# Kernel tuning notes

Hardware: AMD Instinct MI355X
Metric: run time of the kernel (lower is better)

Reference implementation:

```python
import jax, jax.numpy as jnp
import numpy as np

NUM_HEADS = 8


def _mha(x, w_in, b_in, w_out, b_out, nh=NUM_HEADS):
    # x: [B, L, H]; torch nn.MultiheadAttention (batch_first) self-attention
    B, L, H = x.shape
    dh = H // nh
    qkv = x @ w_in.T + b_in                      # [B, L, 3H]
    q, k, v = jnp.split(qkv, 3, axis=-1)
    def heads(t):
        return t.reshape(B, L, nh, dh).transpose(0, 2, 1, 3)  # [B, nh, L, dh]
    q, k, v = heads(q), heads(k), heads(v)
    scale = 1.0 / np.sqrt(dh)
    scores = jnp.einsum('bhqd,bhkd->bhqk', q * scale, k)      # [B, nh, L, L]
    attn = jax.nn.softmax(scores, axis=-1)
    out = jnp.einsum('bhqk,bhkd->bhqd', attn, v)               # [B, nh, L, dh]
    out = out.transpose(0, 2, 1, 3).reshape(B, L, H)
    return out @ w_out.T + b_out


def setup_inputs() -> dict:
    key = jax.random.key(0)
    ks = jax.random.split(key, 10)
    S, M, B, H = 64, 4, 128, 1024
    std = 0.02
    inp = {
        'hidden_states_combined': jax.random.normal(ks[0], (S, M, B, 1, H), jnp.float32),
        'mf_in_w': jax.random.normal(ks[1], (3 * H, H), jnp.float32) * std,
        'mf_in_b': jnp.zeros((3 * H,), jnp.float32),
        'mf_out_w': jax.random.normal(ks[2], (H, H), jnp.float32) * std,
        'mf_out_b': jnp.zeros((H,), jnp.float32),
        'sf_in_w': jax.random.normal(ks[3], (3 * H, H), jnp.float32) * std,
        'sf_in_b': jnp.zeros((3 * H,), jnp.float32),
        'sf_out_w': jax.random.normal(ks[4], (H, H), jnp.float32) * std,
        'sf_out_b': jnp.zeros((H,), jnp.float32),
        'pos_enc': jax.random.normal(ks[5], (1, S, H), jnp.float32) * std,
    }
    return inp


def reference(hidden_states_combined, mf_in_w, mf_in_b, mf_out_w, mf_out_b,
              sf_in_w, sf_in_b, sf_out_w, sf_out_b, pos_enc):
    S, M, B, _, H = hidden_states_combined.shape
    # [S, M, B, 1, H] -> [S, B, M, H] -> batch all steps together: [S*B, M, H]
    x = hidden_states_combined[:, :, :, 0, :].transpose(0, 2, 1, 3).reshape(S * B, M, H)
    fused = _mha(x, mf_in_w, mf_in_b, mf_out_w, mf_out_b)        # [S*B, M, H]
    fused = fused.mean(axis=1).reshape(S, B, H)                  # mean over models
    seq = fused.transpose(1, 0, 2) + pos_enc[:, :S, :]            # [B, S, H]
    enhanced = _mha(seq, sf_in_w, sf_in_b, sf_out_w, sf_out_b)   # [B, S, H]
    return enhanced.transpose(1, 0, 2)[:, :, None, :]             # [S, B, 1, H]
```

## Files before the change

### kernel.cpp

```cpp
#include <hip/hip_runtime.h>

typedef unsigned short u16;
typedef __attribute__((ext_vector_type(8))) short bf16x8;
typedef __attribute__((ext_vector_type(4))) float f32x4;

__device__ __forceinline__ u16 f2bf(float f) {
  unsigned u = __float_as_uint(f);
  u += 0x7FFFu + ((u >> 16) & 1u);
  return (u16)(u >> 16);
}
__device__ __forceinline__ float bf2f(u16 h) {
  return __uint_as_float(((unsigned)h) << 16);
}

#define GLOAD16(g, l) __builtin_amdgcn_global_load_lds( \
    (const __attribute__((address_space(1))) void*)(g), \
    (__attribute__((address_space(3))) void*)(l), 16, 0, 0)

__global__ __launch_bounds__(256) void cvtw4_kernel(const float* __restrict__ s0, u16* __restrict__ d0,
                                                    const float* __restrict__ s1, u16* __restrict__ d1,
                                                    const float* __restrict__ s2, u16* __restrict__ d2,
                                                    const float* __restrict__ s3, u16* __restrict__ d3) {
  int i = blockIdx.x * 256 + threadIdx.x;
  const float* s; u16* d; int off;
  if (i < 786432)       { s = s0; d = d0; off = i; }
  else if (i < 1048576) { s = s1; d = d1; off = i - 786432; }
  else if (i < 1835008) { s = s2; d = d2; off = i - 1048576; }
  else                  { s = s3; d = d3; off = i - 1835008; }
  float4 f = ((const float4*)s)[off];
  ushort4 u;
  u.x = f2bf(f.x); u.y = f2bf(f.y); u.z = f2bf(f.z); u.w = f2bf(f.w);
  ((ushort4*)d)[off] = u;
}

__global__ __launch_bounds__(256) void xcvt_kernel(const float* __restrict__ hidden,
                                                   u16* __restrict__ xb, int s0) {
  int idx = blockIdx.x * 256 + threadIdx.x;
  int h4 = idx & 255;
  int lrow = idx >> 8;
  int m = lrow & 3;
  int b = (lrow >> 2) & 127;
  int sl = lrow >> 9;
  int s = s0 + sl;
  const float4 f = *(const float4*)(hidden + (((size_t)(s * 4 + m) * 128 + b) * 1024) + h4 * 4);
  ushort4 u;
  u.x = f2bf(f.x); u.y = f2bf(f.y); u.z = f2bf(f.z); u.w = f2bf(f.w);
  *(ushort4*)(xb + (size_t)lrow * 1024 + h4 * 4) = u;
}

template <int KK>
__global__ __launch_bounds__(512, 2) void gemm4p(const u16* __restrict__ A,
                                                 const u16* __restrict__ Bw,
                                                 const float* __restrict__ bias,
                                                 u16* __restrict__ C, int N) {
  __shared__ u16 Sh[65536];
  const int t = threadIdx.x, w = t >> 6, l = t & 63;
  const int lr = l & 15, lg = l >> 4;
  const int wm = w >> 2, wn = w & 3;

  const int gx = gridDim.x;
  const int nb = gx * gridDim.y;
  const int id = blockIdx.y * gx + blockIdx.x;
  const int id2 = (id & 7) * (nb >> 3) + (id >> 3);
  const int rowBase = (id2 / gx) * 256, colBase = (id2 % gx) * 256;

  const int sslot8 = ((t & 3) ^ ((t >> 3) & 3)) * 8;
  const u16* Ag = A + (size_t)(rowBase + (t >> 2)) * KK + sslot8;
  const u16* Bg = Bw + (size_t)(colBase + (t >> 2)) * KK + sslot8;
  const size_t K128 = (size_t)128 * KK;
  const int ldsW = w * 512;

  const int fslot8 = (lg ^ ((lr >> 1) & 3)) * 8;
  const int aRowOff = (wm * 128 + lr) * 32 + fslot8;
  const int bRowOff = (wn * 64 + lr) * 32 + fslot8;

  f32x4 acc[8][4];
#pragma unroll
  for (int i = 0; i < 8; i++)
#pragma unroll
    for (int j = 0; j < 4; j++) acc[i][j] = (f32x4){0.f, 0.f, 0.f, 0.f};
  bf16x8 af[2][8], bfr[2][4];

#define STGA(tt, KH, DB) { \
    const u16* g_ = Ag + (size_t)(tt) * 64 + (KH) * 32; \
    GLOAD16(g_, Sh + ((DB) * 2 + (KH)) * 8192 + ldsW); \
    GLOAD16(g_ + K128, Sh + ((DB) * 2 + (KH)) * 8192 + 4096 + ldsW); }
#define STGB(tt, KH, DB) { \
    const u16* g_ = Bg + (size_t)(tt) * 64 + (KH) * 32; \
    GLOAD16(g_, Sh + 32768 + ((DB) * 2 + (KH)) * 8192 + ldsW); \
    GLOAD16(g_ + K128, Sh + 32768 + ((DB) * 2 + (KH)) * 8192 + 4096 + ldsW); }

#define RA8(DD, KH, BUF) { \
    const u16* sa_ = Sh + ((DD) * 2 + (KH)) * 8192 + aRowOff; \
    _Pragma("unroll") \
    for (int mi = 0; mi < 8; mi++) af[BUF][mi] = *(const bf16x8*)(sa_ + mi * 512); }
#define RB4(DD, KH, BUF) { \
    const u16* sb_ = Sh + 32768 + ((DD) * 2 + (KH)) * 8192 + bRowOff; \
    _Pragma("unroll") \
    for (int n = 0; n < 4; n++) bfr[BUF][n] = *(const bf16x8*)(sb_ + n * 512); }

#define LG(NN) asm volatile("s_waitcnt lgkmcnt(" #NN ")" ::: "memory"); \
               __builtin_amdgcn_sched_barrier(0)
#define WTC(NN) asm volatile("s_waitcnt vmcnt(" #NN ")" ::: "memory")
#define BAR asm volatile("s_barrier" ::: "memory")

#define MM32(BUF) { \
    __builtin_amdgcn_s_setprio(1); \
    _Pragma("unroll") \
    for (int mi = 0; mi < 8; mi++) { \
      _Pragma("unroll") \
      for (int n = 0; n < 4; n++) \
        acc[mi][n] = __builtin_amdgcn_mfma_f32_16x16x32_bf16( \
            af[BUF][mi], bfr[BUF][n], acc[mi][n], 0, 0, 0); \
    } \
    __builtin_amdgcn_s_setprio(0); }

  STGA(0, 0, 0); STGB(0, 0, 0);
  STGA(0, 1, 0); STGB(0, 1, 0);
  STGA(1, 0, 1); STGB(1, 0, 1);
  WTC(4);
  BAR;
  RA8(0, 0, 0); RB4(0, 0, 0);

  const int nt = KK / 64;
  for (int tt = 0; tt < nt; ++tt) {
    const int dd = tt & 1;
    RA8(dd, 1, 1); RB4(dd, 1, 1);
    if (tt + 1 < nt) { STGA(tt + 1, 1, dd ^ 1); STGB(tt + 1, 1, dd ^ 1); }
    LG(12);
    MM32(0);
    if (tt + 1 < nt) { WTC(4); }
    BAR;
    if (tt + 1 < nt) {
      RA8(dd ^ 1, 0, 0); RB4(dd ^ 1, 0, 0);
      if (tt + 2 < nt) { STGA(tt + 2, 0, dd); STGB(tt + 2, 0, dd); }
      LG(12);
    } else {
      LG(0);
    }
    MM32(1);
    if (tt + 2 < nt) { WTC(4); }
    else if (tt + 1 < nt) { WTC(0); }
    BAR;
  }
#undef MM32
#undef BAR
#undef WTC
#undef LG
#undef RB4
#undef RA8
#undef STGB
#undef STGA

  const int orow0 = rowBase + wm * 128 + lg * 4;
  const int ocol0 = colBase + wn * 64 + lr;
#pragma unroll
  for (int m = 0; m < 8; m++) {
#pragma unroll
    for (int n = 0; n < 4; n++) {
      const int col = ocol0 + n * 16;
      const float bv = bias[col];
#pragma unroll
      for (int r = 0; r < 4; r++) {
        const int row = orow0 + m * 16 + r;
        C[(size_t)row * N + col] = f2bf(acc[m][n][r] + bv);
      }
    }
  }
}

template <int MODE>
__global__ __launch_bounds__(256, 2) void gemm_fp(const u16* __restrict__ A,
                                                  const u16* __restrict__ Bw,
                                                  const float* __restrict__ bias,
                                                  void* __restrict__ Cout,
                                                  int N, int K,
                                                  const float* __restrict__ posenc) {
  __shared__ u16 SA[3][8192];
  __shared__ u16 SB[3][4096];
  const int t = threadIdx.x, w = t >> 6, l = t & 63;
  const int lr = l & 15, lg = l >> 4;
  const int wm = w >> 1, wn = w & 1;

  const int gx = gridDim.x;
  const int nb = gx * gridDim.y;
  const int id = blockIdx.y * gx + blockIdx.x;
  const int id2 = (id & 7) * (nb >> 3) + (id >> 3);
  const int rowBase = (id2 / gx) * 256, colBase = (id2 % gx) * 128;

  const int srow = l >> 2;
  const int ssl = ((l & 3) ^ (srow & 3)) * 8;
  const u16* Ag = A + (size_t)(rowBase + w * 16 + srow) * K + ssl;
  const u16* Bg = Bw + (size_t)(colBase + w * 16 + srow) * K + ssl;
  u16* const lA = &SA[0][0] + w * 512;
  u16* const lB = &SB[0][0] + w * 512;

  const int fsw = (lg ^ (lr & 3)) * 8;
  const int aoff = (wm * 128 + lr) * 32 + fsw;
  const int boff = (wn * 64 + lr) * 32 + fsw;

  f32x4 acc[8][4];
#pragma unroll
  for (int i = 0; i < 8; i++)
#pragma unroll
    for (int j = 0; j < 4; j++) acc[i][j] = (f32x4){0.f, 0.f, 0.f, 0.f};

#define STG_P0(tt, bb) do { \
    const size_t ko_ = (size_t)(tt) * 32; \
    GLOAD16(Ag + ko_,                    lA + (bb) * 8192); \
    GLOAD16(Ag + ko_ + (size_t)64 * K,   lA + (bb) * 8192 + 2048); \
    GLOAD16(Ag + ko_ + (size_t)128 * K,  lA + (bb) * 8192 + 4096); \
  } while (0)
#define STG_P1(tt, bb) do { \
    const size_t ko_ = (size_t)(tt) * 32; \
    GLOAD16(Ag + ko_ + (size_t)192 * K,  lA + (bb) * 8192 + 6144); \
    GLOAD16(Bg + ko_,                    lB + (bb) * 4096); \
    GLOAD16(Bg + ko_ + (size_t)64 * K,   lB + (bb) * 4096 + 2048); \
  } while (0)
#define FBAR asm volatile("s_barrier" ::: "memory")

  const int nt = K >> 5;
  STG_P0(0, 0); STG_P1(0, 0);
  STG_P0(1, 1); STG_P1(1, 1);
  asm volatile("s_waitcnt vmcnt(6)" ::: "memory");
  FBAR;

  int bcur = 0;
  for (int tt = 0; tt < nt; ++tt) {
    const u16* pa = &SA[bcur][0];
    const u16* pb = &SB[bcur][0];
    const int bnext = (bcur + 2 > 2) ? bcur - 1 : bcur + 2;
    bf16x8 af[4], bfr[4];

#pragma unroll
    for (int m = 0; m < 4; m++) af[m] = *(const bf16x8*)(pa + aoff + m * 512);
#pragma unroll
    for (int n = 0; n < 4; n++) bfr[n] = *(const bf16x8*)(pb + boff + n * 512);
    if (tt + 2 < nt) STG_P0(tt + 2, bnext);
    FBAR;
    asm volatile("s_waitcnt lgkmcnt(0)" ::: "memory");
    __builtin_amdgcn_sched_barrier(0);
    __builtin_amdgcn_s_setprio(1);
#pragma unroll
    for (int m = 0; m < 4; m++)
#pragma unroll
      for (int n = 0; n < 4; n++)
        acc[m][n] = __builtin_amdgcn_mfma_f32_16x16x32_bf16(af[m], bfr[n], acc[m][n], 0, 0, 0);
    __builtin_amdgcn_s_setprio(0);
    FBAR;

#pragma unroll
    for (int m = 0; m < 4; m++) af[m] = *(const bf16x8*)(pa + aoff + (m + 4) * 512);
    if (tt + 2 < nt) STG_P1(tt + 2, bnext);
    FBAR;
    asm volatile("s_waitcnt lgkmcnt(0)" ::: "memory");
    __builtin_amdgcn_sched_barrier(0);
    __builtin_amdgcn_s_setprio(1);
#pragma unroll
    for (int m = 0; m < 4; m++)
#pragma unroll
      for (int n = 0; n < 4; n++)
        acc[m + 4][n] = __builtin_amdgcn_mfma_f32_16x16x32_bf16(af[m], bfr[n], acc[m + 4][n], 0, 0, 0);
    __builtin_amdgcn_s_setprio(0);
    if (tt + 2 < nt) {
      asm volatile("s_waitcnt vmcnt(6)" ::: "memory");
    } else if (tt + 1 < nt) {
      asm volatile("s_waitcnt vmcnt(0)" ::: "memory");
    }
    FBAR;
    bcur = (bcur + 1 > 2) ? 0 : bcur + 1;
  }
#undef FBAR
#undef STG_P0
#undef STG_P1

  const int orow0 = rowBase + wm * 128 + lg * 4;
  const int ocol0 = colBase + wn * 64 + lr;
#pragma unroll
  for (int m = 0; m < 8; m++) {
#pragma unroll
    for (int n = 0; n < 4; n++) {
      const int col = ocol0 + n * 16;
      const float bv = bias[col];
#pragma unroll
      for (int r = 0; r < 4; r++) {
        const int row = orow0 + m * 16 + r;
        float v = acc[m][n][r] + bv;
        if (MODE == 1) {
          int s = row >> 7, b = row & 127;
          v += posenc[s * 1024 + col];
          ((u16*)Cout)[((size_t)(b * 64 + s)) * 1024 + col] = f2bf(v);
        } else {
          int s = row & 63, b = row >> 6;
          ((float*)Cout)[((size_t)(s * 128 + b)) * 1024 + col] = v;
        }
      }
    }
  }
}

__global__ __launch_bounds__(256) void attn1_kernel(const u16* __restrict__ qkv,
                                                    u16* __restrict__ am, int seqBase) {
  const int w = threadIdx.x >> 6, l = threadIdx.x & 63;
  const int pair = blockIdx.x * 4 + w;
  const int seq = pair >> 3, head = pair & 7;
  const int d0 = l * 2;
  const u16* base = qkv + (size_t)(seq * 4) * 3072 + head * 128 + d0;
  const float scale = 0.08838834764831845f;
  float q[4][2], k[4][2], v[4][2];
#pragma unroll
  for (int m = 0; m < 4; m++) {
    ushort2 uq = *(const ushort2*)(base + (size_t)m * 3072);
    ushort2 uk = *(const ushort2*)(base + (size_t)m * 3072 + 1024);
    ushort2 uv = *(const ushort2*)(base + (size_t)m * 3072 + 2048);
    q[m][0] = bf2f(uq.x) * scale; q[m][1] = bf2f(uq.y) * scale;
    k[m][0] = bf2f(uk.x);         k[m][1] = bf2f(uk.y);
    v[m][0] = bf2f(uv.x);         v[m][1] = bf2f(uv.y);
  }
  float sc[4][4];
#pragma unroll
  for (int i = 0; i < 4; i++)
#pragma unroll
    for (int j = 0; j < 4; j++)
      sc[i][j] = q[i][0] * k[j][0] + q[i][1] * k[j][1];
#pragma unroll
  for (int off = 32; off >= 1; off >>= 1)
#pragma unroll
    for (int i = 0; i < 4; i++)
#pragma unroll
      for (int j = 0; j < 4; j++)
        sc[i][j] += __shfl_xor(sc[i][j], off, 64);
  float pbar[4] = {0.f, 0.f, 0.f, 0.f};
#pragma unroll
  for (int i = 0; i < 4; i++) {
    float mx = fmaxf(fmaxf(sc[i][0], sc[i][1]), fmaxf(sc[i][2], sc[i][3]));
    float e0 = __expf(sc[i][0] - mx), e1 = __expf(sc[i][1] - mx);
    float e2 = __expf(sc[i][2] - mx), e3 = __expf(sc[i][3] - mx);
    float inv = 0.25f / (e0 + e1 + e2 + e3);
    pbar[0] += e0 * inv; pbar[1] += e1 * inv; pbar[2] += e2 * inv; pbar[3] += e3 * inv;
  }
  float o0 = pbar[0] * v[0][0] + pbar[1] * v[1][0] + pbar[2] * v[2][0] + pbar[3] * v[3][0];
  float o1 = pbar[0] * v[0][1] + pbar[1] * v[1][1] + pbar[2] * v[2][1] + pbar[3] * v[3][1];
  ushort2 ou; ou.x = f2bf(o0); ou.y = f2bf(o1);
  *(ushort2*)(am + (size_t)(seqBase + seq) * 1024 + head * 128 + d0) = ou;
}

__global__ __launch_bounds__(256) void attn2_kernel(const u16* __restrict__ qkv2,
                                                    u16* __restrict__ aout) {
  __shared__ u16 Qs[64 * 128];
  __shared__ u16 Ks[64 * 128];
  __shared__ u16 Vt[128 * 72];
  __shared__ u16 Ps[64 * 72];
  const int t = threadIdx.x, w = t >> 6, l = t & 63;
  const int lr = l & 15, lg = l >> 4;
  const int b = blockIdx.x >> 3, head = blockIdx.x & 7;
  const u16* qb = qkv2 + (size_t)(b * 64) * 3072 + head * 128;

#pragma unroll
  for (int c = 0; c < 4; c++) {
    int flat = c * 256 + t;
    int row = flat >> 4, sp = flat & 15;
    int sg = (sp ^ (row & 7)) * 8;
    GLOAD16(qb + (size_t)row * 3072 + sg, Qs + (c * 256 + w * 64) * 8);
    GLOAD16(qb + 1024 + (size_t)row * 3072 + sg, Ks + (c * 256 + w * 64) * 8);
  }
  const int dd = (t & 63) * 2, kb = t >> 6;
#pragma unroll
  for (int c = 0; c < 16; c++) {
    int k = c * 4 + kb;
    ushort2 vv = *(const ushort2*)(qb + 2048 + (size_t)k * 3072 + dd);
    Vt[(size_t)dd * 72 + k] = vv.x;
    Vt[(size_t)(dd + 1) * 72 + k] = vv.y;
  }
  __syncthreads();

  f32x4 sc[4];
#pragma unroll
  for (int cb = 0; cb < 4; cb++) sc[cb] = (f32x4){0.f, 0.f, 0.f, 0.f};
#pragma unroll
  for (int ks = 0; ks < 4; ks++) {
    bf16x8 aq = *(const bf16x8*)(Qs + (w * 16 + lr) * 128 + ((ks * 4 + lg) ^ (lr & 7)) * 8);
#pragma unroll
    for (int cb = 0; cb < 4; cb++) {
      bf16x8 bk = *(const bf16x8*)(Ks + (cb * 16 + lr) * 128 + ((ks * 4 + lg) ^ (lr & 7)) * 8);
      sc[cb] = __builtin_amdgcn_mfma_f32_16x16x32_bf16(aq, bk, sc[cb], 0, 0, 0);
    }
  }

  const float scale = 0.08838834764831845f;
#pragma unroll
  for (int r = 0; r < 4; r++) {
#pragma unroll
    for (int cb = 0; cb < 4; cb++) sc[cb][r] *= scale;
    float mx = fmaxf(fmaxf(sc[0][r], sc[1][r]), fmaxf(sc[2][r], sc[3][r]));
#pragma unroll
    for (int off = 1; off < 16; off <<= 1) mx = fmaxf(mx, __shfl_xor(mx, off, 64));
    float sum = 0.f;
#pragma unroll
    for (int cb = 0; cb < 4; cb++) {
      float e = __expf(sc[cb][r] - mx);
      sum += e;
      sc[cb][r] = e;
    }
#pragma unroll
    for (int off = 1; off < 16; off <<= 1) sum += __shfl_xor(sum, off, 64);
    float inv = 1.f / sum;
    int prow = w * 16 + lg * 4 + r;
#pragma unroll
    for (int cb = 0; cb < 4; cb++)
      Ps[(size_t)prow * 72 + cb * 16 + lr] = f2bf(sc[cb][r] * inv);
  }

  f32x4 o[8];
#pragma unroll
  for (int cb = 0; cb < 8; cb++) o[cb] = (f32x4){0.f, 0.f, 0.f, 0.f};
#pragma unroll
  for (int ks = 0; ks < 2; ks++) {
    bf16x8 ap = *(const bf16x8*)(Ps + (w * 16 + lr) * 72 + ks * 32 + lg * 8);
#pragma unroll
    for (int cb = 0; cb < 8; cb++) {
      bf16x8 bv = *(const bf16x8*)(Vt + (cb * 16 + lr) * 72 + ks * 32 + lg * 8);
      o[cb] = __builtin_amdgcn_mfma_f32_16x16x32_bf16(ap, bv, o[cb], 0, 0, 0);
    }
  }
#pragma unroll
  for (int cb = 0; cb < 8; cb++) {
#pragma unroll
    for (int r = 0; r < 4; r++) {
      int srow = w * 16 + lg * 4 + r;
      int d = cb * 16 + lr;
      aout[(size_t)(b * 64 + srow) * 1024 + head * 128 + d] = f2bf(o[cb][r]);
    }
  }
}

extern "C" void kernel_launch(void* const* d_in, const int* in_sizes, int n_in,
                              void* d_out, int out_size, void* d_ws, size_t ws_size,
                              hipStream_t stream) {
  const float* hidden   = (const float*)d_in[0];
  const float* mf_in_w  = (const float*)d_in[1];
  const float* mf_in_b  = (const float*)d_in[2];
  const float* mf_out_w = (const float*)d_in[3];
  const float* mf_out_b = (const float*)d_in[4];
  const float* sf_in_w  = (const float*)d_in[5];
  const float* sf_in_b  = (const float*)d_in[6];
  const float* sf_out_w = (const float*)d_in[7];
  const float* sf_out_b = (const float*)d_in[8];
  const float* pos_enc  = (const float*)d_in[9];

  char* ws = (char*)d_ws;
  u16* w_mf_in  = (u16*)(ws);
  u16* w_mf_out = (u16*)(ws + 6291456);
  u16* w_sf_in  = (u16*)(ws + 8388608);
  u16* w_sf_out = (u16*)(ws + 14680064);

  cvtw4_kernel<<<8192, 256, 0, stream>>>(mf_in_w, w_mf_in, mf_out_w, w_mf_out,
                                         sf_in_w, w_sf_in, sf_out_w, w_sf_out);

  if (ws_size >= 201326592ull) {
    u16* xchunk   = (u16*)(ws + 16777216);
    u16* qkvbuf   = (u16*)(ws + 50331648);
    u16* attnmean = (u16*)(ws + 150994944);
    u16* seqbuf   = (u16*)(ws + 167772160);
    u16* a2out    = (u16*)(ws + 184549376);

    for (int c = 0; c < 2; ++c) {
      xcvt_kernel<<<16384, 256, 0, stream>>>(hidden, xchunk, c * 32);
      gemm4p<1024><<<dim3(12, 64), 512, 0, stream>>>(xchunk, w_mf_in, mf_in_b, qkvbuf, 3072);
      attn1_kernel<<<8192, 256, 0, stream>>>(qkvbuf, attnmean, c * 4096);
    }

    gemm_fp<1><<<dim3(8, 32), 256, 0, stream>>>(attnmean, w_mf_out, mf_out_b, seqbuf,
                                                1024, 1024, pos_enc);
    gemm4p<1024><<<dim3(12, 32), 512, 0, stream>>>(seqbuf, w_sf_in, sf_in_b, qkvbuf, 3072);
    attn2_kernel<<<1024, 256, 0, stream>>>(qkvbuf, a2out);
    gemm_fp<2><<<dim3(8, 32), 256, 0, stream>>>(a2out, w_sf_out, sf_out_b, d_out,
                                                1024, 1024, nullptr);
  } else {
    u16* xchunk   = (u16*)(ws + 16777216);
    u16* qkvbuf   = (u16*)(ws + 33554432);
    u16* attnmean = (u16*)(ws + 83886080);
    u16* seqbuf   = (u16*)(ws + 100663296);
    u16* a2out    = (u16*)(ws + 117440512);

    for (int c = 0; c < 4; ++c) {
      xcvt_kernel<<<8192, 256, 0, stream>>>(hidden, xchunk, c * 16);
      gemm4p<1024><<<dim3(12, 32), 512, 0, stream>>>(xchunk, w_mf_in, mf_in_b, qkvbuf, 3072);
      attn1_kernel<<<4096, 256, 0, stream>>>(qkvbuf, attnmean, c * 2048);
    }

    gemm_fp<1><<<dim3(8, 32), 256, 0, stream>>>(attnmean, w_mf_out, mf_out_b, seqbuf,
                                                1024, 1024, pos_enc);
    gemm4p<1024><<<dim3(12, 32), 512, 0, stream>>>(seqbuf, w_sf_in, sf_in_b, qkvbuf, 3072);
    attn2_kernel<<<1024, 256, 0, stream>>>(qkvbuf, a2out);
    gemm_fp<2><<<dim3(8, 32), 256, 0, stream>>>(a2out, w_sf_out, sf_out_b, d_out,
                                                1024, 1024, nullptr);
  }
}
```

Before: 467.7 us.

## Stage gemm4p epilogue through swizzled LDS and process full batch unchunked

The gemm4p epilogue now writes bias-added bf16 results into a swizzled shared-memory tile and then stores them to global memory as 16-byte row-contiguous vectors, replacing scattered 2-byte stores. The host path also drops the two-chunk loop when the workspace is at least 320 MiB and runs conversion, the QKV GEMM and the first attention over the whole batch in one launch each. This aims to cut uncoalesced-store overhead and launch/tail costs. It needs a larger workspace, and if that is unavailable the older chunked path runs. It also assumes the Sh buffer can be reused after the main loop.

```diff
diff --git a/kernel.cpp b/kernel.cpp
--- a/kernel.cpp
+++ b/kernel.cpp
@@ -144,29 +144,42 @@
     BAR;
   }
 #undef MM32
-#undef BAR
-#undef WTC
-#undef LG
 #undef RB4
 #undef RA8
 #undef STGB
 #undef STGA
 
-  const int orow0 = rowBase + wm * 128 + lg * 4;
-  const int ocol0 = colBase + wn * 64 + lr;
-#pragma unroll
-  for (int m = 0; m < 8; m++) {
-#pragma unroll
-    for (int n = 0; n < 4; n++) {
-      const int col = ocol0 + n * 16;
-      const float bv = bias[col];
-#pragma unroll
-      for (int r = 0; r < 4; r++) {
-        const int row = orow0 + m * 16 + r;
-        C[(size_t)row * N + col] = f2bf(acc[m][n][r] + bv);
+  {
+    const int erow0 = wm * 128 + lg * 4;
+    const int ecol0 = wn * 64 + lr;
+#pragma unroll
+    for (int m = 0; m < 8; m++) {
+#pragma unroll
+      for (int n = 0; n < 4; n++) {
+        const int c = ecol0 + n * 16;
+        const float bv = bias[colBase + c];
+#pragma unroll
+        for (int r = 0; r < 4; r++) {
+          const int row = erow0 + m * 16 + r;
+          const int cs = (((c >> 3) ^ ((row >> 2) & 7)) << 3) | (c & 7);
+          Sh[row * 256 + cs] = f2bf(acc[m][n][r] + bv);
+        }
       }
     }
-  }
+    BAR;
+    const int g = t & 31;
+    const int rsub = t >> 5;
+#pragma unroll
+    for (int pass = 0; pass < 16; pass++) {
+      const int row = pass * 16 + rsub;
+      const int gs = g ^ ((row >> 2) & 7);
+      bf16x8 v = *(const bf16x8*)(Sh + row * 256 + gs * 8);
+      *(bf16x8*)(&C[(size_t)(rowBase + row) * N + colBase + g * 8]) = v;
+    }
+  }
+#undef BAR
+#undef WTC
+#undef LG
 }
 
 template <int MODE>
@@ -457,23 +470,21 @@
   cvtw4_kernel<<<8192, 256, 0, stream>>>(mf_in_w, w_mf_in, mf_out_w, w_mf_out,
                                          sf_in_w, w_sf_in, sf_out_w, w_sf_out);
 
-  if (ws_size >= 201326592ull) {
-    u16* xchunk   = (u16*)(ws + 16777216);
-    u16* qkvbuf   = (u16*)(ws + 50331648);
-    u16* attnmean = (u16*)(ws + 150994944);
-    u16* seqbuf   = (u16*)(ws + 167772160);
-    u16* a2out    = (u16*)(ws + 184549376);
-
-    for (int c = 0; c < 2; ++c) {
-      xcvt_kernel<<<16384, 256, 0, stream>>>(hidden, xchunk, c * 32);
-      gemm4p<1024><<<dim3(12, 64), 512, 0, stream>>>(xchunk, w_mf_in, mf_in_b, qkvbuf, 3072);
-      attn1_kernel<<<8192, 256, 0, stream>>>(qkvbuf, attnmean, c * 4096);
-    }
+  if (ws_size >= 335544320ull) {
+    u16* xfull    = (u16*)(ws + 16777216);
+    u16* qkvfull  = (u16*)(ws + 83886080);
+    u16* attnmean = (u16*)(ws + 285212672);
+    u16* seqbuf   = (u16*)(ws + 301989888);
+    u16* a2out    = (u16*)(ws + 318767104);
+
+    xcvt_kernel<<<32768, 256, 0, stream>>>(hidden, xfull, 0);
+    gemm4p<1024><<<dim3(12, 128), 512, 0, stream>>>(xfull, w_mf_in, mf_in_b, qkvfull, 3072);
+    attn1_kernel<<<16384, 256, 0, stream>>>(qkvfull, attnmean, 0);
 
     gemm_fp<1><<<dim3(8, 32), 256, 0, stream>>>(attnmean, w_mf_out, mf_out_b, seqbuf,
                                                 1024, 1024, pos_enc);
-    gemm4p<1024><<<dim3(12, 32), 512, 0, stream>>>(seqbuf, w_sf_in, sf_in_b, qkvbuf, 3072);
-    attn2_kernel<<<1024, 256, 0, stream>>>(qkvbuf, a2out);
+    gemm4p<1024><<<dim3(12, 32), 512, 0, stream>>>(seqbuf, w_sf_in, sf_in_b, qkvfull, 3072);
+    attn2_kernel<<<1024, 256, 0, stream>>>(qkvfull, a2out);
     gemm_fp<2><<<dim3(8, 32), 256, 0, stream>>>(a2out, w_sf_out, sf_out_b, d_out,
                                                 1024, 1024, nullptr);
   } else {
```

Measured after the change: 477.3 us. 2.0% more time.

## Fuse fp32-to-bf16 input conversion into QKV GEMM and drop chunking

Applied to the files above, without the earlier changes.

Adds a GEMM variant that reads the fp32 hidden states directly with the permuted [S,M,B] row indexing, converts to bf16 in registers and writes the tile to LDS, so the separate xcvt pass and its bf16 staging buffer go away. The large-workspace path also processes all 64 steps in one GEMM launch and one attention launch instead of two chunks, which needs a 256MB workspace. In exchange, the A operand is loaded through registers at twice the bytes instead of via direct global-to-LDS loads, adding register pressure and conversion work inside the main loop. Whether this path runs depends on the harness providing at least 256MB of workspace; otherwise the unchanged fallback path is used.

```diff
diff --git a/kernel.cpp b/kernel.cpp
--- a/kernel.cpp
+++ b/kernel.cpp
@@ -1,6 +1,7 @@
 #include <hip/hip_runtime.h>
 
 typedef unsigned short u16;
+typedef unsigned int u32;
 typedef __attribute__((ext_vector_type(8))) short bf16x8;
 typedef __attribute__((ext_vector_type(4))) float f32x4;
 
@@ -46,6 +47,151 @@
   ushort4 u;
   u.x = f2bf(f.x); u.y = f2bf(f.y); u.z = f2bf(f.z); u.w = f2bf(f.w);
   *(ushort4*)(xb + (size_t)lrow * 1024 + h4 * 4) = u;
+}
+
+template <int KK>
+__global__ __launch_bounds__(512, 2) void gemm4pF(const float* __restrict__ hidden,
+                                                  const u16* __restrict__ Bw,
+                                                  const float* __restrict__ bias,
+                                                  u16* __restrict__ C, int N) {
+  __shared__ u16 Sh[65536];
+  const int t = threadIdx.x, w = t >> 6, l = t & 63;
+  const int lr = l & 15, lg = l >> 4;
+  const int wm = w >> 2, wn = w & 3;
+
+  const int gx = gridDim.x;
+  const int nb = gx * gridDim.y;
+  const int id = blockIdx.y * gx + blockIdx.x;
+  const int id2 = (id & 7) * (nb >> 3) + (id >> 3);
+  const int rowBase = (id2 / gx) * 256, colBase = (id2 % gx) * 256;
+
+  const int srow0 = t >> 2;
+  const int r0 = rowBase + srow0, r1 = r0 + 128;
+  const float* Af0 = hidden + ((size_t)(((r0 >> 9) * 4 + (r0 & 3)) * 128 + ((r0 >> 2) & 127))) * 1024 + (t & 3) * 8;
+  const float* Af1 = hidden + ((size_t)(((r1 >> 9) * 4 + (r1 & 3)) * 128 + ((r1 >> 2) & 127))) * 1024 + (t & 3) * 8;
+  const int wA0 = srow0 * 32 + (((t & 3) ^ ((srow0 >> 1) & 3)) * 8);
+  const int wA1 = wA0 + 128 * 32;
+
+  const int sslot8 = ((t & 3) ^ ((t >> 3) & 3)) * 8;
+  const u16* Bg = Bw + (size_t)(colBase + (t >> 2)) * KK + sslot8;
+  const size_t K128 = (size_t)128 * KK;
+  const int ldsW = w * 512;
+
+  const int fslot8 = (lg ^ ((lr >> 1) & 3)) * 8;
+  const int aRowOff = (wm * 128 + lr) * 32 + fslot8;
+  const int bRowOff = (wn * 64 + lr) * 32 + fslot8;
+
+  f32x4 acc[8][4];
+#pragma unroll
+  for (int i = 0; i < 8; i++)
+#pragma unroll
+    for (int j = 0; j < 4; j++) acc[i][j] = (f32x4){0.f, 0.f, 0.f, 0.f};
+  bf16x8 af[2][8], bfr[2][4];
+  float4 sa0, sa1, sa2, sa3;
+
+#define ALOAD(tt, KH) { \
+    const size_t ko_ = (size_t)(tt) * 64 + (KH) * 32; \
+    sa0 = *(const float4*)(Af0 + ko_);      sa1 = *(const float4*)(Af0 + ko_ + 4); \
+    sa2 = *(const float4*)(Af1 + ko_);      sa3 = *(const float4*)(Af1 + ko_ + 4); }
+#define ACVTW(KH, DB) { \
+    u32 q0, q1, q2, q3, q4, q5, q6, q7; \
+    asm("v_cvt_pk_bf16_f32 %0, %1, %2" : "=v"(q0) : "v"(sa0.x), "v"(sa0.y)); \
+    asm("v_cvt_pk_bf16_f32 %0, %1, %2" : "=v"(q1) : "v"(sa0.z), "v"(sa0.w)); \
+    asm("v_cvt_pk_bf16_f32 %0, %1, %2" : "=v"(q2) : "v"(sa1.x), "v"(sa1.y)); \
+    asm("v_cvt_pk_bf16_f32 %0, %1, %2" : "=v"(q3) : "v"(sa1.z), "v"(sa1.w)); \
+    asm("v_cvt_pk_bf16_f32 %0, %1, %2" : "=v"(q4) : "v"(sa2.x), "v"(sa2.y)); \
+    asm("v_cvt_pk_bf16_f32 %0, %1, %2" : "=v"(q5) : "v"(sa2.z), "v"(sa2.w)); \
+    asm("v_cvt_pk_bf16_f32 %0, %1, %2" : "=v"(q6) : "v"(sa3.x), "v"(sa3.y)); \
+    asm("v_cvt_pk_bf16_f32 %0, %1, %2" : "=v"(q7) : "v"(sa3.z), "v"(sa3.w)); \
+    uint4 u0_ = {q0, q1, q2, q3}, u1_ = {q4, q5, q6, q7}; \
+    u16* dst_ = Sh + ((DB) * 2 + (KH)) * 8192; \
+    *(uint4*)(dst_ + wA0) = u0_; \
+    *(uint4*)(dst_ + wA1) = u1_; }
+#define STGB(tt, KH, DB) { \
+    const u16* g_ = Bg + (size_t)(tt) * 64 + (KH) * 32; \
+    GLOAD16(g_, Sh + 32768 + ((DB) * 2 + (KH)) * 8192 + ldsW); \
+    GLOAD16(g_ + K128, Sh + 32768 + ((DB) * 2 + (KH)) * 8192 + 4096 + ldsW); }
+
+#define RA8(DD, KH, BUF) { \
+    const u16* sa_ = Sh + ((DD) * 2 + (KH)) * 8192 + aRowOff; \
+    _Pragma("unroll") \
+    for (int mi = 0; mi < 8; mi++) af[BUF][mi] = *(const bf16x8*)(sa_ + mi * 512); }
+#define RB4(DD, KH, BUF) { \
+    const u16* sb_ = Sh + 32768 + ((DD) * 2 + (KH)) * 8192 + bRowOff; \
+    _Pragma("unroll") \
+    for (int n = 0; n < 4; n++) bfr[BUF][n] = *(const bf16x8*)(sb_ + n * 512); }
+
+#define LG(NN) asm volatile("s_waitcnt lgkmcnt(" #NN ")" ::: "memory"); \
+               __builtin_amdgcn_sched_barrier(0)
+#define WTC(NN) asm volatile("s_waitcnt vmcnt(" #NN ")" ::: "memory")
+#define BAR asm volatile("s_barrier" ::: "memory")
+
+#define MM32(BUF) { \
+    __builtin_amdgcn_s_setprio(1); \
+    _Pragma("unroll") \
+    for (int mi = 0; mi < 8; mi++) { \
+      _Pragma("unroll") \
+      for (int n = 0; n < 4; n++) \
+        acc[mi][n] = __builtin_amdgcn_mfma_f32_16x16x32_bf16( \
+            af[BUF][mi], bfr[BUF][n], acc[mi][n], 0, 0, 0); \
+    } \
+    __builtin_amdgcn_s_setprio(0); }
+
+  ALOAD(0, 0); WTC(0); ACVTW(0, 0);
+  ALOAD(0, 1); WTC(0); ACVTW(1, 0);
+  ALOAD(1, 0); WTC(0); ACVTW(0, 1);
+  STGB(0, 0, 0); STGB(0, 1, 0); STGB(1, 0, 1);
+  WTC(2);
+  LG(0);
+  BAR;
+  RA8(0, 0, 0); RB4(0, 0, 0);
+
+  const int nt = KK / 64;
+  for (int tt = 0; tt < nt; ++tt) {
+    const int dd = tt & 1;
+    RA8(dd, 1, 1); RB4(dd, 1, 1);
+    if (tt + 1 < nt) { ALOAD(tt + 1, 1); STGB(tt + 1, 1, dd ^ 1); }
+    LG(12);
+    MM32(0);
+    if (tt + 1 < nt) { WTC(2); ACVTW(1, dd ^ 1); }
+    BAR;
+    if (tt + 1 < nt) {
+      RA8(dd ^ 1, 0, 0); RB4(dd ^ 1, 0, 0);
+      if (tt + 2 < nt) { ALOAD(tt + 2, 0); STGB(tt + 2, 0, dd); }
+      LG(12);
+    } else {
+      LG(0);
+    }
+    MM32(1);
+    if (tt + 2 < nt) { WTC(2); ACVTW(0, dd); }
+    else if (tt + 1 < nt) { WTC(0); }
+    BAR;
+  }
+#undef MM32
+#undef BAR
+#undef WTC
+#undef LG
+#undef RB4
+#undef RA8
+#undef STGB
+#undef ACVTW
+#undef ALOAD
+
+  const int orow0 = rowBase + wm * 128 + lg * 4;
+  const int ocol0 = colBase + wn * 64 + lr;
+#pragma unroll
+  for (int m = 0; m < 8; m++) {
+#pragma unroll
+    for (int n = 0; n < 4; n++) {
+      const int col = ocol0 + n * 16;
+      const float bv = bias[col];
+#pragma unroll
+      for (int r = 0; r < 4; r++) {
+        const int row = orow0 + m * 16 + r;
+        C[(size_t)row * N + col] = f2bf(acc[m][n][r] + bv);
+      }
+    }
+  }
 }
 
 template <int KK>
@@ -457,23 +603,19 @@
   cvtw4_kernel<<<8192, 256, 0, stream>>>(mf_in_w, w_mf_in, mf_out_w, w_mf_out,
                                          sf_in_w, w_sf_in, sf_out_w, w_sf_out);
 
-  if (ws_size >= 201326592ull) {
-    u16* xchunk   = (u16*)(ws + 16777216);
-    u16* qkvbuf   = (u16*)(ws + 50331648);
-    u16* attnmean = (u16*)(ws + 150994944);
-    u16* seqbuf   = (u16*)(ws + 167772160);
-    u16* a2out    = (u16*)(ws + 184549376);
-
-    for (int c = 0; c < 2; ++c) {
-      xcvt_kernel<<<16384, 256, 0, stream>>>(hidden, xchunk, c * 32);
-      gemm4p<1024><<<dim3(12, 64), 512, 0, stream>>>(xchunk, w_mf_in, mf_in_b, qkvbuf, 3072);
-      attn1_kernel<<<8192, 256, 0, stream>>>(qkvbuf, attnmean, c * 4096);
-    }
+  if (ws_size >= 268435456ull) {
+    u16* qkvfull  = (u16*)(ws + 16777216);
+    u16* attnmean = (u16*)(ws + 218103808);
+    u16* seqbuf   = (u16*)(ws + 234881024);
+    u16* a2out    = (u16*)(ws + 251658240);
+
+    gemm4pF<1024><<<dim3(12, 128), 512, 0, stream>>>(hidden, w_mf_in, mf_in_b, qkvfull, 3072);
+    attn1_kernel<<<16384, 256, 0, stream>>>(qkvfull, attnmean, 0);
 
     gemm_fp<1><<<dim3(8, 32), 256, 0, stream>>>(attnmean, w_mf_out, mf_out_b, seqbuf,
                                                 1024, 1024, pos_enc);
-    gemm4p<1024><<<dim3(12, 32), 512, 0, stream>>>(seqbuf, w_sf_in, sf_in_b, qkvbuf, 3072);
-    attn2_kernel<<<1024, 256, 0, stream>>>(qkvbuf, a2out);
+    gemm4p<1024><<<dim3(12, 32), 512, 0, stream>>>(seqbuf, w_sf_in, sf_in_b, qkvfull, 3072);
+    attn2_kernel<<<1024, 256, 0, stream>>>(qkvfull, a2out);
     gemm_fp<2><<<dim3(8, 32), 256, 0, stream>>>(a2out, w_sf_out, sf_out_b, d_out,
                                                 1024, 1024, nullptr);
   } else {
```

After: 517.9 us. 1.11x slower.
